# Optimization experiments

Measured on AMD Instinct MI355X. Metric: run time of the kernel, lower is better.

The kernel has to match this reference:

```python
import jax, jax.numpy as jnp
import numpy as np

N_WAY, K_SHOT = 5, 1
N_CLASSES = 64
D = 8


def _conv(x, w, b):
    y = jax.lax.conv_general_dilated(x, w, (2, 2), 'SAME',
                                     dimension_numbers=('NCHW', 'OIHW', 'NCHW'))
    return jax.nn.relu(y + b[None, :, None, None])


def setup_inputs() -> dict:
    key = jax.random.key(0)
    ks = jax.random.split(key, 12)
    b, s_sup, q, h, w = 4, N_WAY * K_SHOT, 1, 64, 64
    rnd = lambda k, shape: jax.random.normal(k, shape, jnp.float32) * 0.05
    return {
        'support_x': jax.random.normal(ks[0], (b, s_sup, 3, h, w), jnp.float32),
        'support_y': jax.random.randint(ks[1], (b, s_sup), 0, N_CLASSES),
        'query_x': jax.random.normal(ks[2], (b, q, 3, h, w), jnp.float32),
        'query_y': jax.random.randint(ks[3], (b, q), 0, N_CLASSES),
        'k1': rnd(ks[4], (32, 3, 3, 3)), 'bc1': jnp.zeros((32,), jnp.float32),
        'k2': rnd(ks[5], (48, 32, 3, 3)), 'bc2': jnp.zeros((48,), jnp.float32),
        'k3': rnd(ks[6], (64, 48, 3, 3)), 'bc3': jnp.zeros((64,), jnp.float32),
        'Wlog': rnd(ks[7], (64, N_CLASSES)), 'blog': jnp.zeros((N_CLASSES,), jnp.float32),
        'Wg1': rnd(ks[8], (132, 128)), 'bg1': jnp.zeros((128,), jnp.float32),
        'Wg2': rnd(ks[9], (128, 64)), 'bg2': jnp.zeros((64,), jnp.float32),
        'Wf1': rnd(ks[10], (64, 16)), 'bf1': jnp.zeros((16,), jnp.float32),
        'Wf2': rnd(ks[11], (16, 1)), 'bf2': jnp.zeros((1,), jnp.float32),
    }


def reference(support_x, support_y, query_x, query_y,
              k1, bc1, k2, bc2, k3, bc3, Wlog, blog,
              Wg1, bg1, Wg2, bg2, Wf1, bf1, Wf2, bf2):
    x = jnp.concatenate([support_x, query_x], axis=1)       # [b, s, 3, h, w]
    label = jnp.concatenate([support_y, query_y], axis=1)   # [b, s]
    b, s = label.shape
    h, w = x.shape[-2:]

    feat = x.reshape(b * s, 3, h, w)
    feat = _conv(feat, k1, bc1)
    feat = _conv(feat, k2, bc2)
    feat = _conv(feat, k3, bc3)                              # [b*s, c, D, D]
    c = feat.shape[1]
    logits = feat.mean(axis=(2, 3)) @ Wlog + blog            # [b*s, n_classes]

    # --- append normalized (i/d, j/d) coord channels ---
    ii = jnp.arange(D, dtype=feat.dtype) / D
    coord = jnp.stack([jnp.broadcast_to(ii[:, None], (D, D)),
                       jnp.broadcast_to(ii[None, :], (D, D))])        # [2, D, D]
    feat = feat.reshape(b, s, c, D, D)
    feat = jnp.concatenate([feat, jnp.broadcast_to(coord, (b, s, 2, D, D))], axis=2)
    c2 = c + 2
    m = D * D
    a = feat.reshape(b, s, c2, m).transpose(0, 1, 3, 2)      # [b, s, m, c2]

    # --- relation network g over all (set-pair, position-pair) combos ---
    # original: g(concat(x_i, x_j)) where x_i = x[b, j, :, q], x_j = x[b, i, :, p]
    # split first linear: concat @ Wg1 = x_i @ Wg1[:c2] + x_j @ Wg1[c2:]
    W1a, W1b = Wg1[:c2], Wg1[c2:]
    u = a @ W1a                                              # [b, s_j, m_q, 128]
    v = a @ W1b + bg1                                        # [b, s_i, m_p, 128]
    # hdd[b,i,j,q,p] = relu(u[b,j,q] + v[b,i,p])  -> [b, s, s, m, m, 128]
    hdd = jax.nn.relu(u[:, None, :, :, None, :] + v[:, :, None, None, :, :])
    g = jax.nn.relu(hdd @ Wg2 + bg2)                         # [b, s, s, m, m, 64]
    x_f = g.sum(axis=(3, 4))                                 # [b, s, s, 64]
    score = jax.nn.sigmoid(jax.nn.relu(x_f @ Wf1 + bf1) @ Wf2 + bf2)  # [b, s, s, 1]

    # --- losses ---
    logp = jax.nn.log_softmax(logits, axis=-1)
    lab = label.reshape(-1)
    cls_loss = -jnp.take_along_axis(logp, lab[:, None], axis=1).mean()

    y = (label[:, :, None] == label[:, None, :])[..., None].astype(score.dtype)
    P = score[..., 0]                                        # [b, s, s]
    Pt = P.transpose(0, 2, 1)
    sym, anti = 0.5 * (P + Pt), 0.5 * (P - Pt)
    sym_n = jnp.sqrt((sym ** 2).sum(axis=(1, 2)))            # Frobenius per batch
    anti_n = jnp.sqrt((anti ** 2).sum(axis=(1, 2)))
    sym_loss = ((sym_n - anti_n) / (sym_n + anti_n)).mean()
    euc_loss = ((score - y) ** 2).mean()
    rn_loss = euc_loss - 0.1 * sym_loss
    return (cls_loss, rn_loss, sym_loss)
```

## Files before the change

### kernel.cpp

```cpp
#include <hip/hip_runtime.h>

typedef _Float16 f16x8 __attribute__((ext_vector_type(8)));
typedef float f32x4 __attribute__((ext_vector_type(4)));

__device__ unsigned g_rel_done = 0;
__device__ unsigned g_c2[24] = {};
__device__ unsigned g_c3[24] = {};


__global__ void __launch_bounds__(256) conv1_k(
        const float* __restrict__ sx, const float* __restrict__ qx,
        const float* __restrict__ w, const float* __restrict__ bias,
        float* __restrict__ out,
        const float* __restrict__ Wg2, _Float16* __restrict__ W2h) {
    if (blockIdx.x == 768) {
        for (int s = 0; s < 4; s++) {
            int slot = threadIdx.x + 256*s;
            int tile = slot >> 6, lane = slot & 63;
            int kt = tile >> 2, nt = tile & 3;
            int quad = lane >> 4, col = lane & 15;
            f16x8 t;
            #pragma unroll
            for (int jj = 0; jj < 8; jj++)
                t[jj] = (_Float16)Wg2[(kt*32 + quad*8 + jj)*64 + nt*16 + col];
            *(f16x8*)&W2h[slot*8] = t;
        }
        return;
    }
    int r8 = blockIdx.x & 7, q = blockIdx.x >> 3;
    int n  = (q >> 5)*8 + r8;
    int oc = q & 31;
    int bi = n / 6, si = n % 6;
    const float* inp = (si < 5) ? sx + (size_t)((bi*5+si)*3)*4096
                                : qx + (size_t)(bi*3)*4096;
    __shared__ __align__(16) float ish[3*4352];
    __shared__ float wl[27];
    __shared__ float bl;
    const int tid = threadIdx.x;
    #pragma unroll
    for (int j = 0; j < 12; j++) {
        int k = tid + j*256;
        f32x4 t = *(const f32x4*)&inp[k*4];
        int plane = k >> 10, rem = k & 1023, row = rem >> 4, c4 = (rem & 15)*4;
        *(f32x4*)&ish[plane*4352 + row*68 + c4] = t;
    }
    if (tid < 27) wl[tid] = w[oc*27 + tid];
    if (tid == 31) bl = bias[oc];
    __syncthreads();
    for (int idx = tid; idx < 1024; idx += 256) {
        int oy = idx >> 5, ox = idx & 31;
        float acc = bl;
        #pragma unroll
        for (int ic = 0; ic < 3; ic++) {
            const float* ip = &ish[ic*4352];
            #pragma unroll
            for (int dy = 0; dy < 3; dy++) {
                int iy = 2*oy + dy;
                if (iy >= 64) continue;
                #pragma unroll
                for (int dx = 0; dx < 3; dx++) {
                    int ix = 2*ox + dx;
                    if (ix >= 64) continue;
                    acc += ip[iy*68+ix] * wl[ic*9 + dy*3 + dx];
                }
            }
        }
        out[(size_t)(n*32+oc)*1024 + idx] = fmaxf(acc, 0.f);
    }
}

__global__ void __launch_bounds__(256) fused_k(
        const float* __restrict__ feat1, const float* __restrict__ k2w,
        const float* __restrict__ bc2, float* __restrict__ feat2,
        const float* __restrict__ k3w, const float* __restrict__ bc3,
        float* __restrict__ feat3g, float* __restrict__ mf,
        const float* __restrict__ Wg1, const float* __restrict__ bg1,
        _Float16* __restrict__ u16, _Float16* __restrict__ v16,
        const int* __restrict__ sy, const int* __restrict__ qy,
        const float* __restrict__ Wlog, const float* __restrict__ blog,
        float* __restrict__ rv) {
    __shared__ __align__(16) float smem[19584];
    __shared__ unsigned Rsh;
    const int tid = threadIdx.x;

    int r8 = blockIdx.x & 7, q = blockIdx.x >> 3;
    int n = (q / 12)*8 + r8;
    int L = q % 12;

    {
        float* wl  = smem;
        float* pin = smem + 1152;
        const float* ib = feat1 + (size_t)n*32*1024;
        #pragma unroll
        for (int j = 0; j < 16; j++) {
            int k = tid + j*256;
            f32x4 t = *(const f32x4*)&ib[k*4];
            int s = k >> 8, rem = k & 255, row = rem >> 3, c4 = (rem & 7)*4;
            *(f32x4*)&pin[s*1152 + row*36 + c4] = t;
        }
        f32x4 rb[16];
        #pragma unroll
        for (int j = 0; j < 16; j++) {
            int k = tid + j*256;
            rb[j] = *(const f32x4*)&ib[16384 + k*4];
        }
        for (int e = tid; e < 288; e += 256)
            *(f32x4*)&wl[e*4] = *(const f32x4*)&k2w[L*1152 + e*4];
        __syncthreads();
        int oy = tid >> 4, ox = tid & 15;
        float a0 = bc2[L*4+0], a1 = bc2[L*4+1];
        float a2 = bc2[L*4+2], a3 = bc2[L*4+3];
        #pragma unroll 4
        for (int ic = 0; ic < 16; ic++) {
            const float* pp = &pin[ic*1152];
            float tap[9];
            #pragma unroll
            for (int dy = 0; dy < 3; dy++)
                #pragma unroll
                for (int dx = 0; dx < 3; dx++) {
                    int iy = 2*oy+dy, ix = 2*ox+dx;
                    tap[dy*3+dx] = (iy < 32 && ix < 32) ? pp[iy*36 + ix] : 0.f;
                }
            #pragma unroll
            for (int t = 0; t < 9; t++) {
                a0 += tap[t]*wl[0*288 + ic*9 + t];
                a1 += tap[t]*wl[1*288 + ic*9 + t];
                a2 += tap[t]*wl[2*288 + ic*9 + t];
                a3 += tap[t]*wl[3*288 + ic*9 + t];
            }
        }
        __syncthreads();
        #pragma unroll
        for (int j = 0; j < 16; j++) {
            int k = tid + j*256;
            int s = k >> 8, rem = k & 255, row = rem >> 3, c4 = (rem & 7)*4;
            *(f32x4*)&pin[s*1152 + row*36 + c4] = rb[j];
        }
        __syncthreads();
        #pragma unroll 4
        for (int ic = 16; ic < 32; ic++) {
            const float* pp = &pin[(ic-16)*1152];
            float tap[9];
            #pragma unroll
            for (int dy = 0; dy < 3; dy++)
                #pragma unroll
                for (int dx = 0; dx < 3; dx++) {
                    int iy = 2*oy+dy, ix = 2*ox+dx;
                    tap[dy*3+dx] = (iy < 32 && ix < 32) ? pp[iy*36 + ix] : 0.f;
                }
            #pragma unroll
            for (int t = 0; t < 9; t++) {
                a0 += tap[t]*wl[0*288 + ic*9 + t];
                a1 += tap[t]*wl[1*288 + ic*9 + t];
                a2 += tap[t]*wl[2*288 + ic*9 + t];
                a3 += tap[t]*wl[3*288 + ic*9 + t];
            }
        }
        size_t ob = (size_t)(n*48 + L*4)*256 + tid;
        __hip_atomic_store(&feat2[ob      ], fmaxf(a0, 0.f), __ATOMIC_RELAXED, __HIP_MEMORY_SCOPE_AGENT);
        __hip_atomic_store(&feat2[ob + 256], fmaxf(a1, 0.f), __ATOMIC_RELAXED, __HIP_MEMORY_SCOPE_AGENT);
        __hip_atomic_store(&feat2[ob + 512], fmaxf(a2, 0.f), __ATOMIC_RELAXED, __HIP_MEMORY_SCOPE_AGENT);
        __hip_atomic_store(&feat2[ob + 768], fmaxf(a3, 0.f), __ATOMIC_RELAXED, __HIP_MEMORY_SCOPE_AGENT);
    }
    asm volatile("s_waitcnt vmcnt(0)" ::: "memory");
    __syncthreads();
    if (tid == 0) {
        unsigned my = __hip_atomic_fetch_add(&g_c2[n], 1u, __ATOMIC_RELAXED,
                                             __HIP_MEMORY_SCOPE_AGENT) + 1u;
        Rsh = (my + 11u) / 12u;
    }
    __syncthreads();
    const unsigned R = Rsh;
    if (L >= 9) return;

    if (L < 8) {
        if (tid == 0) {
            while (__hip_atomic_load(&g_c2[n], __ATOMIC_RELAXED,
                                     __HIP_MEMORY_SCOPE_AGENT) < R*12u)
                __builtin_amdgcn_s_sleep(2);
        }
        __syncthreads();

        float* pin3 = smem;
        float* wl3  = smem + 15360;
        {
            const float* f2 = feat2 + (size_t)n*48*256;
            #pragma unroll 8
            for (int jj = 0; jj < 48; jj++) {
                int k = tid + jj*256;
                float vIn = __hip_atomic_load(&f2[k], __ATOMIC_RELAXED,
                                              __HIP_MEMORY_SCOPE_AGENT);
                int plane = k >> 8, rem = k & 255, row = rem >> 4, cc = rem & 15;
                pin3[plane*320 + row*20 + cc] = vIn;
            }
        }
        for (int e = tid; e < 864; e += 256)
            *(f32x4*)&wl3[e*4] = *(const f32x4*)&k3w[L*3456 + e*4];
        __syncthreads();
        int pix = tid & 63, osub = tid >> 6;
        int oy3 = pix >> 3, ox3 = pix & 7;
        int ol0 = osub*2;
        float a0 = bc3[L*8 + ol0], a1 = bc3[L*8 + ol0 + 1];
        #pragma unroll 4
        for (int ic = 0; ic < 48; ic++) {
            const float* pp = &pin3[ic*320];
            float tap[9];
            #pragma unroll
            for (int dy = 0; dy < 3; dy++)
                #pragma unroll
                for (int dx = 0; dx < 3; dx++) {
                    int iy = 2*oy3+dy, ix = 2*ox3+dx;
                    tap[dy*3+dx] = (iy < 16 && ix < 16) ? pp[iy*20 + ix] : 0.f;
                }
            #pragma unroll
            for (int t = 0; t < 9; t++) {
                a0 += tap[t]*wl3[ ol0   *432 + ic*9 + t];
                a1 += tap[t]*wl3[(ol0+1)*432 + ic*9 + t];
            }
        }
        float r0 = fmaxf(a0, 0.f), r1 = fmaxf(a1, 0.f);
        __hip_atomic_store(&feat3g[(size_t)(n*64 + L*8 + ol0  )*64 + pix], r0,
                           __ATOMIC_RELAXED, __HIP_MEMORY_SCOPE_AGENT);
        __hip_atomic_store(&feat3g[(size_t)(n*64 + L*8 + ol0+1)*64 + pix], r1,
                           __ATOMIC_RELAXED, __HIP_MEMORY_SCOPE_AGENT);
        #pragma unroll
        for (int off = 32; off >= 1; off >>= 1) {
            r0 += __shfl_xor(r0, off, 64);
            r1 += __shfl_xor(r1, off, 64);
        }
        if (pix == 0) {
            __hip_atomic_store(&mf[n*64 + L*8 + ol0    ], r0 * (1.f/64.f),
                               __ATOMIC_RELAXED, __HIP_MEMORY_SCOPE_AGENT);
            __hip_atomic_store(&mf[n*64 + L*8 + ol0 + 1], r1 * (1.f/64.f),
                               __ATOMIC_RELAXED, __HIP_MEMORY_SCOPE_AGENT);
        }
        asm volatile("s_waitcnt vmcnt(0)" ::: "memory");
        __syncthreads();
        if (tid == 0)
            __hip_atomic_fetch_add(&g_c3[n], 1u, __ATOMIC_RELAXED,
                                   __HIP_MEMORY_SCOPE_AGENT);
    }

    if (tid == 0) {
        while (__hip_atomic_load(&g_c3[n], __ATOMIC_RELAXED,
                                 __HIP_MEMORY_SCOPE_AGENT) < R*8u)
            __builtin_amdgcn_s_sleep(2);
    }
    __syncthreads();

    if (L == 8) {
        if (tid < 64) {
            float s = blog[tid];
            for (int c = 0; c < 64; c++)
                s += __hip_atomic_load(&mf[n*64 + c], __ATOMIC_RELAXED,
                                       __HIP_MEMORY_SCOPE_AGENT) * Wlog[c*64 + tid];
            float mx = s;
            #pragma unroll
            for (int off = 32; off >= 1; off >>= 1) mx = fmaxf(mx, __shfl_xor(mx, off, 64));
            float p = __expf(s - mx);
            float se = p;
            #pragma unroll
            for (int off = 32; off >= 1; off >>= 1) se += __shfl_xor(se, off, 64);
            int bi = n/6, si = n%6;
            int lab = (si < 5) ? sy[bi*5+si] : qy[bi];
            float s_lab = __shfl(s, lab, 64);
            if (tid == 0) rv[n] = -(s_lab - mx - __logf(se));
        }
        return;
    }

    {
        int half = tid >> 7, t = tid & 127;
        int pg = L*2 + half;
        float* a4 = smem + half*264;
        for (int e = t; e < 264; e += 128) {
            int pl = e / 66, c = e % 66;
            int p = pg*4 + pl;
            float vv;
            if (c < 64)
                vv = __hip_atomic_load(&feat3g[(size_t)(n*64 + c)*64 + p],
                                       __ATOMIC_RELAXED, __HIP_MEMORY_SCOPE_AGENT);
            else if (c == 64) vv = (float)(p >> 3) * 0.125f;
            else              vv = (float)(p & 7) * 0.125f;
            a4[pl*66 + c] = vv;
        }
        __syncthreads();
        float us[4] = {0.f,0.f,0.f,0.f};
        float bg = bg1[t];
        float vs[4] = {bg,bg,bg,bg};
        for (int c = 0; c < 66; c++) {
            float wa = Wg1[c*128 + t];
            float wb = Wg1[(66+c)*128 + t];
            #pragma unroll
            for (int pl = 0; pl < 4; pl++) {
                us[pl] += a4[pl*66 + c]*wa;
                vs[pl] += a4[pl*66 + c]*wb;
            }
        }
        #pragma unroll
        for (int pl = 0; pl < 4; pl++) {
            int p = pg*4 + pl;
            u16[(size_t)(n*64+p)*128 + t] = (_Float16)us[pl];
            v16[(size_t)(n*64+p)*128 + t] = (_Float16)vs[pl];
        }
    }
}

__global__ void __launch_bounds__(256, 2) rel_k(
        const _Float16* __restrict__ U, const _Float16* __restrict__ V,
        const _Float16* __restrict__ W2h, const float* __restrict__ bg2,
        float* __restrict__ xfpT,
        const float* __restrict__ rv,
        const int* __restrict__ sy, const int* __restrict__ qy,
        const float* __restrict__ Wf1, const float* __restrict__ bf1,
        const float* __restrict__ Wf2, const float* __restrict__ bf2,
        float* __restrict__ out) {
    __shared__ __align__(16) float smem[1792];
    __shared__ unsigned lastflag;
    _Float16* Vsh   = (_Float16*)smem;
    float*    xfred = smem + 1024;

    int r8 = blockIdx.x & 7, qq = blockIdx.x >> 3;
    int b = r8 >> 1;
    int m = (qq << 1) | (r8 & 1);
    int cb = m >> 2, qc = m & 3;
    int j = cb / 6, i = cb % 6;
    int tid  = threadIdx.x;
    int wv   = tid >> 6, lane = tid & 63;
    int col  = lane & 15, quad = lane >> 4;

    const _Float16* ub = U + (size_t)(b*6 + i)*8192;
    const _Float16* vb = V + (size_t)(b*6 + j)*8192 + qc*16*128;

    *(f16x8*)&Vsh[tid*8] = *(const f16x8*)&vb[tid*8];

    f16x8 uf[4];
    {
        const _Float16* up = ub + (wv*16 + col)*128 + quad*8;
        #pragma unroll
        for (int kt = 0; kt < 4; kt++) uf[kt] = *(const f16x8*)&up[kt*32];
    }
    f16x8 bf[4][4];
    #pragma unroll
    for (int kt = 0; kt < 4; kt++)
        #pragma unroll
        for (int nt = 0; nt < 4; nt++)
            bf[kt][nt] = *(const f16x8*)&W2h[(size_t)(((kt*4+nt)*64) + lane)*8];
    float bgv[4];
    #pragma unroll
    for (int nt = 0; nt < 4; nt++) bgv[nt] = bg2[nt*16 + col];

    __syncthreads();

    float sums[4] = {0.f,0.f,0.f,0.f};
    for (int qi = 0; qi < 16; qi++) {
        const _Float16* vp = &Vsh[qi*128 + quad*8];
        f32x4 acc[4];
        #pragma unroll
        for (int nt = 0; nt < 4; nt++)
            acc[nt] = (f32x4){bgv[nt], bgv[nt], bgv[nt], bgv[nt]};
        #pragma unroll
        for (int kt = 0; kt < 4; kt++) {
            f16x8 vf = *(const f16x8*)&vp[kt*32];
            f16x8 af = uf[kt] + vf;
            af = __builtin_elementwise_max(af, (f16x8){0,0,0,0,0,0,0,0});
            #pragma unroll
            for (int nt = 0; nt < 4; nt++)
                acc[nt] = __builtin_amdgcn_mfma_f32_16x16x32_f16(af, bf[kt][nt], acc[nt], 0, 0, 0);
        }
        #pragma unroll
        for (int nt = 0; nt < 4; nt++)
            #pragma unroll
            for (int rr = 0; rr < 4; rr++)
                sums[nt] += fmaxf(acc[nt][rr], 0.f);
    }

    #pragma unroll
    for (int nt = 0; nt < 4; nt++) {
        sums[nt] += __shfl_xor(sums[nt], 16, 64);
        sums[nt] += __shfl_xor(sums[nt], 32, 64);
    }
    if (lane < 16) {
        #pragma unroll
        for (int nt = 0; nt < 4; nt++) xfred[wv*64 + nt*16 + lane] = sums[nt];
    }
    __syncthreads();
    if (tid < 64) {
        float val = xfred[tid] + xfred[64+tid] + xfred[128+tid] + xfred[192+tid];
        __hip_atomic_store(&xfpT[(size_t)tid*576 + (unsigned)(b*144 + m)], val,
                           __ATOMIC_RELAXED, __HIP_MEMORY_SCOPE_AGENT);
    }
    if (wv == 0) asm volatile("s_waitcnt vmcnt(0)" ::: "memory");
    if (tid == 0) {
        unsigned my = __hip_atomic_fetch_add(&g_rel_done, 1u, __ATOMIC_RELAXED,
                                             __HIP_MEMORY_SCOPE_AGENT);
        lastflag = ((my % 576u) == 575u) ? 1u : 0u;
    }
    __syncthreads();
    if (!lastflag) return;

    {
        float* Wf1sh = smem;
        float* wf2sh = smem + 1024;
        float* bf1sh = smem + 1040;
        float* Pm    = smem + 1056;
        int*   lab   = (int*)(smem + 1200);
        float* red   = smem + 1232;
        float* ratio = smem + 1488;
        for (int e = tid; e < 1024; e += 256) Wf1sh[e] = Wf1[e];
        if (tid < 16) { wf2sh[tid] = Wf2[tid]; bf1sh[tid] = bf1[tid]; }
        if (tid < 24) { int bi = tid/6, si = tid%6; lab[tid] = (si < 5) ? sy[bi*5+si] : qy[bi]; }
        __syncthreads();
        if (tid < 144) {
            float hid[16];
            #pragma unroll
            for (int h = 0; h < 16; h++) hid[h] = bf1sh[h];
            for (int nn = 0; nn < 64; nn++) {
                const float* xp = &xfpT[(size_t)nn*576 + tid*4];
                float x = 0.f;
                #pragma unroll
                for (int c = 0; c < 4; c++)
                    x += __hip_atomic_load(&xp[c], __ATOMIC_RELAXED,
                                           __HIP_MEMORY_SCOPE_AGENT);
                #pragma unroll
                for (int h = 0; h < 16; h++) hid[h] += x * Wf1sh[nn*16 + h];
            }
            float sc = bf2[0];
            #pragma unroll
            for (int h = 0; h < 16; h++) sc += fmaxf(hid[h], 0.f) * wf2sh[h];
            Pm[tid] = 1.f/(1.f + __expf(-sc));
        }
        __syncthreads();
        float e = 0.f;
        if (tid < 144) {
            int bb = tid/36, r = tid%36, jj = r/6, ii = r%6;
            float y = (lab[bb*6+jj] == lab[bb*6+ii]) ? 1.f : 0.f;
            float d = Pm[tid] - y;
            e = d*d;
        }
        red[tid] = e;
        __syncthreads();
        for (int s = 128; s > 0; s >>= 1) {
            if (tid < s) red[tid] += red[tid+s];
            __syncthreads();
        }
        if (tid < 4) {
            float s2 = 0.f, a2 = 0.f;
            for (int jj = 0; jj < 6; jj++)
                for (int ii = 0; ii < 6; ii++) {
                    float pa = Pm[tid*36 + jj*6 + ii], pb = Pm[tid*36 + ii*6 + jj];
                    float sm = 0.5f*(pa+pb), an = 0.5f*(pa-pb);
                    s2 += sm*sm; a2 += an*an;
                }
            float sn = sqrtf(s2), anq = sqrtf(a2);
            ratio[tid] = (sn - anq)/(sn + anq);
        }
        __syncthreads();
        if (tid == 0) {
            float sl = 0.25f*(ratio[0]+ratio[1]+ratio[2]+ratio[3]);
            float euc = red[0] * (1.f/144.f);
            float cs = 0.f;
            for (int k = 0; k < 24; k++) cs += rv[k];
            out[0] = cs * (1.f/24.f);
            out[1] = euc - 0.1f*sl;
            out[2] = sl;
        }
    }
}

extern "C" void kernel_launch(void* const* d_in, const int* in_sizes, int n_in,
                              void* d_out, int out_size, void* d_ws, size_t ws_size,
                              hipStream_t stream) {
    const float* sx   = (const float*)d_in[0];
    const int*   sy   = (const int*)  d_in[1];
    const float* qx   = (const float*)d_in[2];
    const int*   qy   = (const int*)  d_in[3];
    const float* k1   = (const float*)d_in[4];
    const float* bc1  = (const float*)d_in[5];
    const float* k2   = (const float*)d_in[6];
    const float* bc2  = (const float*)d_in[7];
    const float* k3   = (const float*)d_in[8];
    const float* bc3  = (const float*)d_in[9];
    const float* Wlog = (const float*)d_in[10];
    const float* blog = (const float*)d_in[11];
    const float* Wg1  = (const float*)d_in[12];
    const float* bg1  = (const float*)d_in[13];
    const float* Wg2  = (const float*)d_in[14];
    const float* bg2  = (const float*)d_in[15];
    const float* Wf1  = (const float*)d_in[16];
    const float* bf1  = (const float*)d_in[17];
    const float* Wf2  = (const float*)d_in[18];
    const float* bf2  = (const float*)d_in[19];

    float* ws    = (float*)d_ws;
    float* feat1 = ws;
    float* feat2 = feat1 + 786432;
    float* feat3 = feat2 + 294912;
    float* mf    = feat3 + 98304;
    float* rv    = mf    + 1536;
    float* xfpT  = rv    + 32;
    _Float16* u16 = (_Float16*)(xfpT + 36864);
    _Float16* v16 = u16 + 196608;
    _Float16* W2h = v16 + 196608;
    float* out   = (float*)d_out;

    conv1_k <<<769,   256, 0, stream>>>(sx, qx, k1, bc1, feat1, Wg2, W2h);
    fused_k <<<24*12, 256, 0, stream>>>(feat1, k2, bc2, feat2, k3, bc3, feat3, mf,
                                        Wg1, bg1, u16, v16, sy, qy, Wlog, blog, rv);
    rel_k   <<<576,   256, 0, stream>>>(u16, v16, W2h, bg2, xfpT,
                                        rv, sy, qy, Wf1, bf1, Wf2, bf2, out);
}
```

Baseline: 171.9 us.

## Split fused conv kernel into separate launches and widen conv1 per-block channels

The fused conv2/conv3 kernel, which synchronized through global counters and spin-waits, is split into a standalone conv2 kernel and a conv3+u/v kernel. The split uses kernel boundaries instead of inter-block barriers, and the logits/loss computation moves to the L==0 block after the u/v projection. conv1 now computes 8 output channels per block from one shared input tile, so the block count drops from 769 to 97 and input reloads are cut. This adds one kernel launch and leaves far fewer conv1 blocks to fill the GPU.

Result: no change. 168.9 us (-1.7%).

```diff
diff --git a/kernel.cpp b/kernel.cpp
--- a/kernel.cpp
+++ b/kernel.cpp
@@ -4,7 +4,6 @@
 typedef float f32x4 __attribute__((ext_vector_type(4)));
 
 __device__ unsigned g_rel_done = 0;
-__device__ unsigned g_c2[24] = {};
 __device__ unsigned g_c3[24] = {};
 
 
@@ -13,7 +12,7 @@
         const float* __restrict__ w, const float* __restrict__ bias,
         float* __restrict__ out,
         const float* __restrict__ Wg2, _Float16* __restrict__ W2h) {
-    if (blockIdx.x == 768) {
+    if (blockIdx.x == 96) {
         for (int s = 0; s < 4; s++) {
             int slot = threadIdx.x + 256*s;
             int tile = slot >> 6, lane = slot & 63;
@@ -28,14 +27,14 @@
         return;
     }
     int r8 = blockIdx.x & 7, q = blockIdx.x >> 3;
-    int n  = (q >> 5)*8 + r8;
-    int oc = q & 31;
+    int n    = (q >> 2)*8 + r8;
+    int oc0  = (q & 3)*8;
     int bi = n / 6, si = n % 6;
     const float* inp = (si < 5) ? sx + (size_t)((bi*5+si)*3)*4096
                                 : qx + (size_t)(bi*3)*4096;
     __shared__ __align__(16) float ish[3*4352];
-    __shared__ float wl[27];
-    __shared__ float bl;
+    __shared__ float wl[216];
+    __shared__ float bl[8];
     const int tid = threadIdx.x;
     #pragma unroll
     for (int j = 0; j < 12; j++) {
@@ -44,230 +43,200 @@
         int plane = k >> 10, rem = k & 1023, row = rem >> 4, c4 = (rem & 15)*4;
         *(f32x4*)&ish[plane*4352 + row*68 + c4] = t;
     }
-    if (tid < 27) wl[tid] = w[oc*27 + tid];
-    if (tid == 31) bl = bias[oc];
-    __syncthreads();
-    for (int idx = tid; idx < 1024; idx += 256) {
+    if (tid < 216) wl[tid] = w[oc0*27 + tid];
+    if (tid >= 240 && tid < 248) bl[tid-240] = bias[oc0 + tid - 240];
+    __syncthreads();
+    for (int s = 0; s < 4; s++) {
+        int idx = tid + s*256;
         int oy = idx >> 5, ox = idx & 31;
-        float acc = bl;
-        #pragma unroll
-        for (int ic = 0; ic < 3; ic++) {
-            const float* ip = &ish[ic*4352];
+        float tap[27];
+        #pragma unroll
+        for (int ic = 0; ic < 3; ic++)
             #pragma unroll
             for (int dy = 0; dy < 3; dy++) {
                 int iy = 2*oy + dy;
-                if (iy >= 64) continue;
                 #pragma unroll
                 for (int dx = 0; dx < 3; dx++) {
                     int ix = 2*ox + dx;
-                    if (ix >= 64) continue;
-                    acc += ip[iy*68+ix] * wl[ic*9 + dy*3 + dx];
+                    tap[ic*9+dy*3+dx] = (iy < 64 && ix < 64)
+                                      ? ish[ic*4352 + iy*68 + ix] : 0.f;
                 }
             }
-        }
-        out[(size_t)(n*32+oc)*1024 + idx] = fmaxf(acc, 0.f);
+        #pragma unroll
+        for (int o = 0; o < 8; o++) {
+            float acc = bl[o];
+            #pragma unroll
+            for (int t = 0; t < 27; t++) acc += tap[t]*wl[o*27 + t];
+            out[(size_t)(n*32 + oc0 + o)*1024 + idx] = fmaxf(acc, 0.f);
+        }
     }
 }
 
-__global__ void __launch_bounds__(256) fused_k(
-        const float* __restrict__ feat1, const float* __restrict__ k2w,
-        const float* __restrict__ bc2, float* __restrict__ feat2,
-        const float* __restrict__ k3w, const float* __restrict__ bc3,
-        float* __restrict__ feat3g, float* __restrict__ mf,
+__global__ void __launch_bounds__(256) conv2_k(
+        const float* __restrict__ in, const float* __restrict__ w,
+        const float* __restrict__ bias, float* __restrict__ out) {
+    int r8 = blockIdx.x & 7, q = blockIdx.x >> 3;
+    int n   = (q / 12)*8 + r8;
+    int ocg = q % 12;
+    __shared__ __align__(16) float wl[1152];
+    __shared__ __align__(16) float pin[16*1152];
+    const int tid = threadIdx.x;
+    const float* ib = in + (size_t)n*32*1024;
+    #pragma unroll
+    for (int j = 0; j < 16; j++) {
+        int k = tid + j*256;
+        f32x4 t = *(const f32x4*)&ib[k*4];
+        int s = k >> 8, rem = k & 255, row = rem >> 3, c4 = (rem & 7)*4;
+        *(f32x4*)&pin[s*1152 + row*36 + c4] = t;
+    }
+    f32x4 rb[16];
+    #pragma unroll
+    for (int j = 0; j < 16; j++) {
+        int k = tid + j*256;
+        rb[j] = *(const f32x4*)&ib[16384 + k*4];
+    }
+    for (int e = tid; e < 288; e += 256)
+        *(f32x4*)&wl[e*4] = *(const f32x4*)&w[ocg*1152 + e*4];
+    __syncthreads();
+    int oy = tid >> 4, ox = tid & 15;
+    float a0 = bias[ocg*4+0], a1 = bias[ocg*4+1];
+    float a2 = bias[ocg*4+2], a3 = bias[ocg*4+3];
+    #pragma unroll 4
+    for (int ic = 0; ic < 16; ic++) {
+        const float* pp = &pin[ic*1152];
+        float tap[9];
+        #pragma unroll
+        for (int dy = 0; dy < 3; dy++)
+            #pragma unroll
+            for (int dx = 0; dx < 3; dx++) {
+                int iy = 2*oy+dy, ix = 2*ox+dx;
+                tap[dy*3+dx] = (iy < 32 && ix < 32) ? pp[iy*36 + ix] : 0.f;
+            }
+        #pragma unroll
+        for (int t = 0; t < 9; t++) {
+            a0 += tap[t]*wl[0*288 + ic*9 + t];
+            a1 += tap[t]*wl[1*288 + ic*9 + t];
+            a2 += tap[t]*wl[2*288 + ic*9 + t];
+            a3 += tap[t]*wl[3*288 + ic*9 + t];
+        }
+    }
+    __syncthreads();
+    #pragma unroll
+    for (int j = 0; j < 16; j++) {
+        int k = tid + j*256;
+        int s = k >> 8, rem = k & 255, row = rem >> 3, c4 = (rem & 7)*4;
+        *(f32x4*)&pin[s*1152 + row*36 + c4] = rb[j];
+    }
+    __syncthreads();
+    #pragma unroll 4
+    for (int ic = 16; ic < 32; ic++) {
+        const float* pp = &pin[(ic-16)*1152];
+        float tap[9];
+        #pragma unroll
+        for (int dy = 0; dy < 3; dy++)
+            #pragma unroll
+            for (int dx = 0; dx < 3; dx++) {
+                int iy = 2*oy+dy, ix = 2*ox+dx;
+                tap[dy*3+dx] = (iy < 32 && ix < 32) ? pp[iy*36 + ix] : 0.f;
+            }
+        #pragma unroll
+        for (int t = 0; t < 9; t++) {
+            a0 += tap[t]*wl[0*288 + ic*9 + t];
+            a1 += tap[t]*wl[1*288 + ic*9 + t];
+            a2 += tap[t]*wl[2*288 + ic*9 + t];
+            a3 += tap[t]*wl[3*288 + ic*9 + t];
+        }
+    }
+    size_t ob = (size_t)(n*48 + ocg*4)*256 + tid;
+    out[ob        ] = fmaxf(a0, 0.f);
+    out[ob + 256  ] = fmaxf(a1, 0.f);
+    out[ob + 512  ] = fmaxf(a2, 0.f);
+    out[ob + 768  ] = fmaxf(a3, 0.f);
+}
+
+__global__ void __launch_bounds__(256) conv3uv_k(
+        const float* __restrict__ feat2, const float* __restrict__ k3w,
+        const float* __restrict__ bc3, float* __restrict__ feat3g,
+        float* __restrict__ mf,
         const float* __restrict__ Wg1, const float* __restrict__ bg1,
         _Float16* __restrict__ u16, _Float16* __restrict__ v16,
         const int* __restrict__ sy, const int* __restrict__ qy,
         const float* __restrict__ Wlog, const float* __restrict__ blog,
         float* __restrict__ rv) {
-    __shared__ __align__(16) float smem[19584];
+    __shared__ __align__(16) float smem[18816];
     __shared__ unsigned Rsh;
     const int tid = threadIdx.x;
-
     int r8 = blockIdx.x & 7, q = blockIdx.x >> 3;
-    int n = (q / 12)*8 + r8;
-    int L = q % 12;
-
+    int n = (q >> 3)*8 + r8;
+    int L = q & 7;
+
+    float* pin3 = smem;
+    float* wl3  = smem + 15360;
     {
-        float* wl  = smem;
-        float* pin = smem + 1152;
-        const float* ib = feat1 + (size_t)n*32*1024;
-        #pragma unroll
-        for (int j = 0; j < 16; j++) {
+        const float* ib = feat2 + (size_t)n*48*256;
+        #pragma unroll
+        for (int j = 0; j < 12; j++) {
             int k = tid + j*256;
             f32x4 t = *(const f32x4*)&ib[k*4];
-            int s = k >> 8, rem = k & 255, row = rem >> 3, c4 = (rem & 7)*4;
-            *(f32x4*)&pin[s*1152 + row*36 + c4] = t;
-        }
-        f32x4 rb[16];
-        #pragma unroll
-        for (int j = 0; j < 16; j++) {
-            int k = tid + j*256;
-            rb[j] = *(const f32x4*)&ib[16384 + k*4];
-        }
-        for (int e = tid; e < 288; e += 256)
-            *(f32x4*)&wl[e*4] = *(const f32x4*)&k2w[L*1152 + e*4];
-        __syncthreads();
-        int oy = tid >> 4, ox = tid & 15;
-        float a0 = bc2[L*4+0], a1 = bc2[L*4+1];
-        float a2 = bc2[L*4+2], a3 = bc2[L*4+3];
-        #pragma unroll 4
-        for (int ic = 0; ic < 16; ic++) {
-            const float* pp = &pin[ic*1152];
-            float tap[9];
-            #pragma unroll
-            for (int dy = 0; dy < 3; dy++)
-                #pragma unroll
-                for (int dx = 0; dx < 3; dx++) {
-                    int iy = 2*oy+dy, ix = 2*ox+dx;
-                    tap[dy*3+dx] = (iy < 32 && ix < 32) ? pp[iy*36 + ix] : 0.f;
-                }
-            #pragma unroll
-            for (int t = 0; t < 9; t++) {
-                a0 += tap[t]*wl[0*288 + ic*9 + t];
-                a1 += tap[t]*wl[1*288 + ic*9 + t];
-                a2 += tap[t]*wl[2*288 + ic*9 + t];
-                a3 += tap[t]*wl[3*288 + ic*9 + t];
+            int plane = k >> 6, rem = k & 63, row = rem >> 2, c4 = (rem & 3)*4;
+            *(f32x4*)&pin3[plane*320 + row*20 + c4] = t;
+        }
+    }
+    for (int e = tid; e < 864; e += 256)
+        *(f32x4*)&wl3[e*4] = *(const f32x4*)&k3w[L*3456 + e*4];
+    __syncthreads();
+    int pix = tid & 63, osub = tid >> 6;
+    int oy = pix >> 3, ox = pix & 7;
+    int ol0 = osub*2;
+    float a0 = bc3[L*8 + ol0], a1 = bc3[L*8 + ol0 + 1];
+    #pragma unroll 4
+    for (int ic = 0; ic < 48; ic++) {
+        const float* pp = &pin3[ic*320];
+        float tap[9];
+        #pragma unroll
+        for (int dy = 0; dy < 3; dy++)
+            #pragma unroll
+            for (int dx = 0; dx < 3; dx++) {
+                int iy = 2*oy+dy, ix = 2*ox+dx;
+                tap[dy*3+dx] = (iy < 16 && ix < 16) ? pp[iy*20 + ix] : 0.f;
             }
-        }
-        __syncthreads();
-        #pragma unroll
-        for (int j = 0; j < 16; j++) {
-            int k = tid + j*256;
-            int s = k >> 8, rem = k & 255, row = rem >> 3, c4 = (rem & 7)*4;
-            *(f32x4*)&pin[s*1152 + row*36 + c4] = rb[j];
-        }
-        __syncthreads();
-        #pragma unroll 4
-        for (int ic = 16; ic < 32; ic++) {
-            const float* pp = &pin[(ic-16)*1152];
-            float tap[9];
-            #pragma unroll
-            for (int dy = 0; dy < 3; dy++)
-                #pragma unroll
-                for (int dx = 0; dx < 3; dx++) {
-                    int iy = 2*oy+dy, ix = 2*ox+dx;
-                    tap[dy*3+dx] = (iy < 32 && ix < 32) ? pp[iy*36 + ix] : 0.f;
-                }
-            #pragma unroll
-            for (int t = 0; t < 9; t++) {
-                a0 += tap[t]*wl[0*288 + ic*9 + t];
-                a1 += tap[t]*wl[1*288 + ic*9 + t];
-                a2 += tap[t]*wl[2*288 + ic*9 + t];
-                a3 += tap[t]*wl[3*288 + ic*9 + t];
-            }
-        }
-        size_t ob = (size_t)(n*48 + L*4)*256 + tid;
-        __hip_atomic_store(&feat2[ob      ], fmaxf(a0, 0.f), __ATOMIC_RELAXED, __HIP_MEMORY_SCOPE_AGENT);
-        __hip_atomic_store(&feat2[ob + 256], fmaxf(a1, 0.f), __ATOMIC_RELAXED, __HIP_MEMORY_SCOPE_AGENT);
-        __hip_atomic_store(&feat2[ob + 512], fmaxf(a2, 0.f), __ATOMIC_RELAXED, __HIP_MEMORY_SCOPE_AGENT);
-        __hip_atomic_store(&feat2[ob + 768], fmaxf(a3, 0.f), __ATOMIC_RELAXED, __HIP_MEMORY_SCOPE_AGENT);
+        #pragma unroll
+        for (int t = 0; t < 9; t++) {
+            a0 += tap[t]*wl3[ ol0   *432 + ic*9 + t];
+            a1 += tap[t]*wl3[(ol0+1)*432 + ic*9 + t];
+        }
+    }
+    float r0 = fmaxf(a0, 0.f), r1 = fmaxf(a1, 0.f);
+    __hip_atomic_store(&feat3g[(size_t)(n*64 + L*8 + ol0  )*64 + pix], r0,
+                       __ATOMIC_RELAXED, __HIP_MEMORY_SCOPE_AGENT);
+    __hip_atomic_store(&feat3g[(size_t)(n*64 + L*8 + ol0+1)*64 + pix], r1,
+                       __ATOMIC_RELAXED, __HIP_MEMORY_SCOPE_AGENT);
+    #pragma unroll
+    for (int off = 32; off >= 1; off >>= 1) {
+        r0 += __shfl_xor(r0, off, 64);
+        r1 += __shfl_xor(r1, off, 64);
+    }
+    if (pix == 0) {
+        __hip_atomic_store(&mf[n*64 + L*8 + ol0    ], r0 * (1.f/64.f),
+                           __ATOMIC_RELAXED, __HIP_MEMORY_SCOPE_AGENT);
+        __hip_atomic_store(&mf[n*64 + L*8 + ol0 + 1], r1 * (1.f/64.f),
+                           __ATOMIC_RELAXED, __HIP_MEMORY_SCOPE_AGENT);
     }
     asm volatile("s_waitcnt vmcnt(0)" ::: "memory");
     __syncthreads();
     if (tid == 0) {
-        unsigned my = __hip_atomic_fetch_add(&g_c2[n], 1u, __ATOMIC_RELAXED,
+        unsigned my = __hip_atomic_fetch_add(&g_c3[n], 1u, __ATOMIC_RELAXED,
                                              __HIP_MEMORY_SCOPE_AGENT) + 1u;
-        Rsh = (my + 11u) / 12u;
+        Rsh = (my + 7u) / 8u;
     }
     __syncthreads();
     const unsigned R = Rsh;
-    if (L >= 9) return;
-
-    if (L < 8) {
-        if (tid == 0) {
-            while (__hip_atomic_load(&g_c2[n], __ATOMIC_RELAXED,
-                                     __HIP_MEMORY_SCOPE_AGENT) < R*12u)
-                __builtin_amdgcn_s_sleep(2);
-        }
-        __syncthreads();
-
-        float* pin3 = smem;
-        float* wl3  = smem + 15360;
-        {
-            const float* f2 = feat2 + (size_t)n*48*256;
-            #pragma unroll 8
-            for (int jj = 0; jj < 48; jj++) {
-                int k = tid + jj*256;
-                float vIn = __hip_atomic_load(&f2[k], __ATOMIC_RELAXED,
-                                              __HIP_MEMORY_SCOPE_AGENT);
-                int plane = k >> 8, rem = k & 255, row = rem >> 4, cc = rem & 15;
-                pin3[plane*320 + row*20 + cc] = vIn;
-            }
-        }
-        for (int e = tid; e < 864; e += 256)
-            *(f32x4*)&wl3[e*4] = *(const f32x4*)&k3w[L*3456 + e*4];
-        __syncthreads();
-        int pix = tid & 63, osub = tid >> 6;
-        int oy3 = pix >> 3, ox3 = pix & 7;
-        int ol0 = osub*2;
-        float a0 = bc3[L*8 + ol0], a1 = bc3[L*8 + ol0 + 1];
-        #pragma unroll 4
-        for (int ic = 0; ic < 48; ic++) {
-            const float* pp = &pin3[ic*320];
-            float tap[9];
-            #pragma unroll
-            for (int dy = 0; dy < 3; dy++)
-                #pragma unroll
-                for (int dx = 0; dx < 3; dx++) {
-                    int iy = 2*oy3+dy, ix = 2*ox3+dx;
-                    tap[dy*3+dx] = (iy < 16 && ix < 16) ? pp[iy*20 + ix] : 0.f;
-                }
-            #pragma unroll
-            for (int t = 0; t < 9; t++) {
-                a0 += tap[t]*wl3[ ol0   *432 + ic*9 + t];
-                a1 += tap[t]*wl3[(ol0+1)*432 + ic*9 + t];
-            }
-        }
-        float r0 = fmaxf(a0, 0.f), r1 = fmaxf(a1, 0.f);
-        __hip_atomic_store(&feat3g[(size_t)(n*64 + L*8 + ol0  )*64 + pix], r0,
-                           __ATOMIC_RELAXED, __HIP_MEMORY_SCOPE_AGENT);
-        __hip_atomic_store(&feat3g[(size_t)(n*64 + L*8 + ol0+1)*64 + pix], r1,
-                           __ATOMIC_RELAXED, __HIP_MEMORY_SCOPE_AGENT);
-        #pragma unroll
-        for (int off = 32; off >= 1; off >>= 1) {
-            r0 += __shfl_xor(r0, off, 64);
-            r1 += __shfl_xor(r1, off, 64);
-        }
-        if (pix == 0) {
-            __hip_atomic_store(&mf[n*64 + L*8 + ol0    ], r0 * (1.f/64.f),
-                               __ATOMIC_RELAXED, __HIP_MEMORY_SCOPE_AGENT);
-            __hip_atomic_store(&mf[n*64 + L*8 + ol0 + 1], r1 * (1.f/64.f),
-                               __ATOMIC_RELAXED, __HIP_MEMORY_SCOPE_AGENT);
-        }
-        asm volatile("s_waitcnt vmcnt(0)" ::: "memory");
-        __syncthreads();
-        if (tid == 0)
-            __hip_atomic_fetch_add(&g_c3[n], 1u, __ATOMIC_RELAXED,
-                                   __HIP_MEMORY_SCOPE_AGENT);
-    }
-
     if (tid == 0) {
         while (__hip_atomic_load(&g_c3[n], __ATOMIC_RELAXED,
                                  __HIP_MEMORY_SCOPE_AGENT) < R*8u)
             __builtin_amdgcn_s_sleep(2);
     }
     __syncthreads();
-
-    if (L == 8) {
-        if (tid < 64) {
-            float s = blog[tid];
-            for (int c = 0; c < 64; c++)
-                s += __hip_atomic_load(&mf[n*64 + c], __ATOMIC_RELAXED,
-                                       __HIP_MEMORY_SCOPE_AGENT) * Wlog[c*64 + tid];
-            float mx = s;
-            #pragma unroll
-            for (int off = 32; off >= 1; off >>= 1) mx = fmaxf(mx, __shfl_xor(mx, off, 64));
-            float p = __expf(s - mx);
-            float se = p;
-            #pragma unroll
-            for (int off = 32; off >= 1; off >>= 1) se += __shfl_xor(se, off, 64);
-            int bi = n/6, si = n%6;
-            int lab = (si < 5) ? sy[bi*5+si] : qy[bi];
-            float s_lab = __shfl(s, lab, 64);
-            if (tid == 0) rv[n] = -(s_lab - mx - __logf(se));
-        }
-        return;
-    }
 
     {
         int half = tid >> 7, t = tid & 127;
@@ -303,6 +272,24 @@
             u16[(size_t)(n*64+p)*128 + t] = (_Float16)us[pl];
             v16[(size_t)(n*64+p)*128 + t] = (_Float16)vs[pl];
         }
+    }
+
+    if (L == 0 && tid < 64) {
+        float s = blog[tid];
+        for (int c = 0; c < 64; c++)
+            s += __hip_atomic_load(&mf[n*64 + c], __ATOMIC_RELAXED,
+                                   __HIP_MEMORY_SCOPE_AGENT) * Wlog[c*64 + tid];
+        float mx = s;
+        #pragma unroll
+        for (int off = 32; off >= 1; off >>= 1) mx = fmaxf(mx, __shfl_xor(mx, off, 64));
+        float p = __expf(s - mx);
+        float se = p;
+        #pragma unroll
+        for (int off = 32; off >= 1; off >>= 1) se += __shfl_xor(se, off, 64);
+        int bi = n/6, si = n%6;
+        int lab = (si < 5) ? sy[bi*5+si] : qy[bi];
+        float s_lab = __shfl(s, lab, 64);
+        if (tid == 0) rv[n] = -(s_lab - mx - __logf(se));
     }
 }
 
@@ -504,9 +491,10 @@
     _Float16* W2h = v16 + 196608;
     float* out   = (float*)d_out;
 
-    conv1_k <<<769,   256, 0, stream>>>(sx, qx, k1, bc1, feat1, Wg2, W2h);
-    fused_k <<<24*12, 256, 0, stream>>>(feat1, k2, bc2, feat2, k3, bc3, feat3, mf,
+    conv1_k   <<<97,  256, 0, stream>>>(sx, qx, k1, bc1, feat1, Wg2, W2h);
+    conv2_k   <<<288, 256, 0, stream>>>(feat1, k2, bc2, feat2);
+    conv3uv_k <<<192, 256, 0, stream>>>(feat2, k3, bc3, feat3, mf,
                                         Wg1, bg1, u16, v16, sy, qy, Wlog, blog, rv);
-    rel_k   <<<576,   256, 0, stream>>>(u16, v16, W2h, bg2, xfpT,
+    rel_k     <<<576, 256, 0, stream>>>(u16, v16, W2h, bg2, xfpT,
                                         rv, sy, qy, Wf1, bf1, Wf2, bf2, out);
 }
```
